# Optimization experiments

Hardware: AMD Instinct MI355X
Metric: run time of the kernel (lower is better)

Reference implementation:

```python
import math
import jax, jax.numpy as jnp
import numpy as np

DIM = 2048
N_HEADS = 16
HEAD_DIM = DIM // N_HEADS  # 128
BSZ = 2
SEQLEN = 2048
ROPE_THETA = 500000.0


def _make_freqs(seqlen, head_dim, theta):
    inv = 1.0 / (theta ** (np.arange(0, head_dim, 2, dtype=np.float32) / head_dim))
    t = np.arange(seqlen, dtype=np.float32)
    f = np.outer(t, inv)  # [S, hd//2]
    return jnp.asarray(np.cos(f)), jnp.asarray(np.sin(f))


def setup_inputs() -> dict:
    key = jax.random.key(0)
    kx, kq, kk, kv, ko = jax.random.split(key, 5)
    scale = 0.02
    x = jax.random.normal(kx, (BSZ, SEQLEN, DIM), dtype=jnp.float32)
    wq = jax.random.normal(kq, (DIM, DIM), dtype=jnp.float32) * scale
    wk = jax.random.normal(kk, (DIM, DIM), dtype=jnp.float32) * scale
    wv = jax.random.normal(kv, (DIM, DIM), dtype=jnp.float32) * scale
    wo = jax.random.normal(ko, (DIM, DIM), dtype=jnp.float32) * scale
    freqs_cos, freqs_sin = _make_freqs(SEQLEN, HEAD_DIM, ROPE_THETA)
    # causal additive mask: 0 on/below diag, -inf above
    mask = jnp.triu(jnp.full((SEQLEN, SEQLEN), float('-inf'), dtype=jnp.float32), k=1)
    return {"x": x, "start_pos": 0, "freqs_cos": freqs_cos, "freqs_sin": freqs_sin,
            "mask": mask, "wq": wq, "wk": wk, "wv": wv, "wo": wo}


def _apply_rope(t, cos, sin):
    # t: [B, S, H, hd]; cos/sin: [S, hd//2]
    b, s, h, hd = t.shape
    tr = t.reshape(b, s, h, hd // 2, 2)
    a, bb = tr[..., 0], tr[..., 1]
    c = cos[None, :, None, :]
    sn = sin[None, :, None, :]
    out_r = a * c - bb * sn
    out_i = a * sn + bb * c
    return jnp.stack([out_r, out_i], axis=-1).reshape(b, s, h, hd)


def reference(x, start_pos, freqs_cos, freqs_sin, mask, wq, wk, wv, wo):
    b, s, _ = x.shape
    xq = (x @ wq.T).reshape(b, s, N_HEADS, HEAD_DIM)
    xk = (x @ wk.T).reshape(b, s, N_HEADS, HEAD_DIM)
    xv = (x @ wv.T).reshape(b, s, N_HEADS, HEAD_DIM)
    xq = _apply_rope(xq, freqs_cos, freqs_sin)
    xk = _apply_rope(xk, freqs_cos, freqs_sin)
    # [B, H, S, hd]
    xq = xq.transpose(0, 2, 1, 3)
    xk = xk.transpose(0, 2, 1, 3)
    xv = xv.transpose(0, 2, 1, 3)
    scores = jnp.einsum('bhqd,bhkd->bhqk', xq, xk) / math.sqrt(HEAD_DIM)
    scores = scores + mask[None, None, :, :]
    probs = jax.nn.softmax(scores.astype(jnp.float32), axis=-1).astype(xq.dtype)
    out = jnp.einsum('bhqk,bhkd->bhqd', probs, xv)
    out = out.transpose(0, 2, 1, 3).reshape(b, s, -1)
    return out @ wo.T
```

## Files before the change

kernel.cpp:

```cpp
#include <hip/hip_runtime.h>
#include <stdint.h>

#define DIM 2048
#define SEQ 2048
#define NHEADS 16
#define HDIM 128
#define BSZ 2
#define ROWS (BSZ*SEQ)

typedef uint16_t u16;
typedef __attribute__((ext_vector_type(8))) short bf16x8;
typedef __attribute__((ext_vector_type(4))) float fx4;
typedef __attribute__((ext_vector_type(4))) uint16_t u16x4;

typedef const __attribute__((address_space(1))) uint32_t* gp_t;
typedef __attribute__((address_space(3))) uint32_t* lp_t;
#define GLL16(g, l) __builtin_amdgcn_global_load_lds((gp_t)(g), (lp_t)(l), 16, 0, 0)

__device__ inline u16 f2bf(float f) {
  union { float f; uint32_t u; } v; v.f = f;
  uint32_t u = v.u;
  u += 0x7FFFu + ((u >> 16) & 1u);
  return (u16)(u >> 16);
}
__device__ inline float bf2f(u16 h) {
  union { uint32_t u; float f; } v; v.u = ((uint32_t)h) << 16;
  return v.f;
}

__global__ __launch_bounds__(256) void cvt_kernel(const float* __restrict__ src,
                                                  u16* __restrict__ dst, int n4) {
  int i = blockIdx.x * 256 + threadIdx.x;
  if (i >= n4) return;
  fx4 f = *(const fx4*)(src + (size_t)i * 4);
  u16x4 o;
  o[0] = f2bf(f[0]); o[1] = f2bf(f[1]); o[2] = f2bf(f[2]); o[3] = f2bf(f[3]);
  *(u16x4*)(dst + (size_t)i * 4) = o;
}

__device__ inline void gemm128_core(const u16* __restrict__ A, const u16* __restrict__ B,
                                    u16 (&As)[128][32], u16 (&Bs)[128][32],
                                    fx4 (&acc)[4][4], int M0, int N0) {
  const int tid  = threadIdx.x;
  const int lane = tid & 63;
  const int wave = tid >> 6;
  const int wm = (wave >> 1) * 64;
  const int wn = (wave & 1) * 64;
  const int l16 = lane & 15;
  const int q8  = (lane >> 4) * 8;
#pragma unroll
  for (int tm = 0; tm < 4; ++tm)
#pragma unroll
    for (int tn = 0; tn < 4; ++tn) acc[tm][tn] = fx4{0.f, 0.f, 0.f, 0.f};

  const int wrow = wave * 32;
  const size_t laneA = (size_t)(M0 + wrow + (lane >> 2)) * DIM + (lane & 3) * 8;
  const size_t laneB = (size_t)(N0 + wrow + (lane >> 2)) * DIM + (lane & 3) * 8;

  for (int k0 = 0; k0 < DIM; k0 += 32) {
    __syncthreads();
    GLL16(A + laneA + k0,            &As[wrow][0]);
    GLL16(A + laneA + 16 * DIM + k0, &As[wrow + 16][0]);
    GLL16(B + laneB + k0,            &Bs[wrow][0]);
    GLL16(B + laneB + 16 * DIM + k0, &Bs[wrow + 16][0]);
    __syncthreads();
    bf16x8 af[4], bfr[4];
#pragma unroll
    for (int t = 0; t < 4; ++t) {
      af[t]  = *(const bf16x8*)&As[wm + t * 16 + l16][q8];
      bfr[t] = *(const bf16x8*)&Bs[wn + t * 16 + l16][q8];
    }
#pragma unroll
    for (int tm = 0; tm < 4; ++tm)
#pragma unroll
      for (int tn = 0; tn < 4; ++tn)
        acc[tm][tn] = __builtin_amdgcn_mfma_f32_16x16x32_bf16(af[tm], bfr[tn], acc[tm][tn], 0, 0, 0);
  }
}

__global__ __launch_bounds__(256) void gemm_qkv(const u16* __restrict__ A,
    const u16* __restrict__ B0, const u16* __restrict__ B1, const u16* __restrict__ B2,
    u16* __restrict__ C0, u16* __restrict__ C1, u16* __restrict__ C2) {
  __shared__ __align__(16) u16 As[128][32];
  __shared__ __align__(16) u16 Bs[128][32];
  const u16* B = (blockIdx.z == 0) ? B0 : (blockIdx.z == 1) ? B1 : B2;
  u16* C       = (blockIdx.z == 0) ? C0 : (blockIdx.z == 1) ? C1 : C2;
  const int M0 = blockIdx.y * 128, N0 = blockIdx.x * 128;
  fx4 acc[4][4];
  gemm128_core(A, B, As, Bs, acc, M0, N0);
  const int lane = threadIdx.x & 63, wave = threadIdx.x >> 6;
  const int wm = (wave >> 1) * 64, wn = (wave & 1) * 64;
  const int l16 = lane & 15, quad = lane >> 4;
#pragma unroll
  for (int tm = 0; tm < 4; ++tm)
#pragma unroll
    for (int tn = 0; tn < 4; ++tn)
#pragma unroll
      for (int r = 0; r < 4; ++r) {
        size_t row = (size_t)(M0 + wm + tm * 16 + quad * 4 + r);
        size_t col = (size_t)(N0 + wn + tn * 16 + l16);
        C[row * DIM + col] = f2bf(acc[tm][tn][r]);
      }
}

__global__ __launch_bounds__(256) void gemm_out(const u16* __restrict__ A,
                                                const u16* __restrict__ B,
                                                float* __restrict__ C) {
  __shared__ __align__(16) u16 As[128][32];
  __shared__ __align__(16) u16 Bs[128][32];
  const int M0 = blockIdx.y * 128, N0 = blockIdx.x * 128;
  fx4 acc[4][4];
  gemm128_core(A, B, As, Bs, acc, M0, N0);
  const int lane = threadIdx.x & 63, wave = threadIdx.x >> 6;
  const int wm = (wave >> 1) * 64, wn = (wave & 1) * 64;
  const int l16 = lane & 15, quad = lane >> 4;
#pragma unroll
  for (int tm = 0; tm < 4; ++tm)
#pragma unroll
    for (int tn = 0; tn < 4; ++tn)
#pragma unroll
      for (int r = 0; r < 4; ++r) {
        size_t row = (size_t)(M0 + wm + tm * 16 + quad * 4 + r);
        size_t col = (size_t)(N0 + wn + tn * 16 + l16);
        C[row * DIM + col] = acc[tm][tn][r];
      }
}

__global__ __launch_bounds__(256) void rope_kernel(u16* __restrict__ q, u16* __restrict__ k,
                                                   const float* __restrict__ fcos,
                                                   const float* __restrict__ fsin) {
  int idx = blockIdx.x * 256 + threadIdx.x;
  int t = idx >> 22;
  int p_all = idx & ((1 << 22) - 1);
  u16* ptr = t ? k : q;
  int row = p_all >> 10;
  int r   = p_all & 1023;
  int h   = r >> 6;
  int p   = r & 63;
  int s   = row & (SEQ - 1);
  size_t base = (size_t)row * DIM + h * HDIM + 2 * p;
  float a = bf2f(ptr[base]), b = bf2f(ptr[base + 1]);
  float c = fcos[s * 64 + p], sn = fsin[s * 64 + p];
  ptr[base]     = f2bf(a * c - b * sn);
  ptr[base + 1] = f2bf(a * sn + b * c);
}

__global__ __launch_bounds__(256) void vtrans_kernel(const u16* __restrict__ v,
                                                     u16* __restrict__ vtg) {
  __shared__ __align__(16) u16 T[128][72];
  const int tid = threadIdx.x;
  const int s0 = blockIdx.x * 64;
  const int bh = blockIdx.y;
  const int b = bh >> 4, h = bh & 15;
  const size_t vb = ((size_t)b * SEQ + s0) * DIM + h * HDIM;
#pragma unroll
  for (int i = 0; i < 4; ++i) {
    int c = i * 256 + tid;
    int s = c >> 4;
    int d0 = (c & 15) * 8;
    bf16x8 x = *(const bf16x8*)(v + vb + (size_t)s * DIM + d0);
#pragma unroll
    for (int j = 0; j < 8; ++j) T[d0 + j][s] = (u16)x[j];
  }
  __syncthreads();
  const size_t ob = ((size_t)bh * HDIM) * SEQ + s0;
#pragma unroll
  for (int i = 0; i < 4; ++i) {
    int c = i * 256 + tid;
    int d = c >> 3;
    int s8 = (c & 7) * 8;
    *(bf16x8*)(vtg + ob + (size_t)d * SEQ + s8) = *(const bf16x8*)&T[d][s8];
  }
}

__global__ __launch_bounds__(256) void attn_kernel(const u16* __restrict__ qm,
                                                   const u16* __restrict__ km,
                                                   const u16* __restrict__ vtg,
                                                   u16* __restrict__ ao) {
  __shared__ __align__(16) u16 Ks[64][136];
  __shared__ __align__(16) u16 Vt[128][72];
  __shared__ __align__(16) u16 Ps[4][16][72];
  const int tid = threadIdx.x;
  const int lane = tid & 63, wave = tid >> 6;
  const int l16 = lane & 15, quad = lane >> 4;
  const int bh = blockIdx.x;
  const int qt = (SEQ / 64 - 1) - blockIdx.y;
  const int b = bh >> 4, h = bh & 15;
  const int q0 = qt * 64;
  const size_t brow = (size_t)b * SEQ;
  const int hc = h * HDIM;
  const size_t vbase = (size_t)bh * HDIM * SEQ;

  bf16x8 aq[4];
  {
    size_t qbase = (brow + q0 + wave * 16 + l16) * DIM + hc;
#pragma unroll
    for (int dc = 0; dc < 4; ++dc)
      aq[dc] = *(const bf16x8*)(qm + qbase + dc * 32 + quad * 8);
  }
  fx4 o[8];
#pragma unroll
  for (int i = 0; i < 8; ++i) o[i] = fx4{0.f, 0.f, 0.f, 0.f};
  float mr[4], lr[4];
#pragma unroll
  for (int r = 0; r < 4; ++r) { mr[r] = -3e38f; lr[r] = 0.f; }

  bf16x8 kreg[4], vreg[4];
#pragma unroll
  for (int i = 0; i < 4; ++i) {
    int c = i * 256 + tid;
    kreg[i] = *(const bf16x8*)(km + (brow + (c >> 4)) * DIM + hc + (c & 15) * 8);
    vreg[i] = *(const bf16x8*)(vtg + vbase + (size_t)(c >> 3) * SEQ + (c & 7) * 8);
  }

  for (int kt = 0; kt <= qt; ++kt) {
    __syncthreads();
#pragma unroll
    for (int i = 0; i < 4; ++i) {
      int c = i * 256 + tid;
      *(bf16x8*)&Ks[c >> 4][(c & 15) * 8] = kreg[i];
      *(bf16x8*)&Vt[c >> 3][(c & 7) * 8] = vreg[i];
    }
    __syncthreads();
    if (kt < qt) {
      const int kv1 = (kt + 1) * 64;
#pragma unroll
      for (int i = 0; i < 4; ++i) {
        int c = i * 256 + tid;
        kreg[i] = *(const bf16x8*)(km + (brow + kv1 + (c >> 4)) * DIM + hc + (c & 15) * 8);
        vreg[i] = *(const bf16x8*)(vtg + vbase + (size_t)(c >> 3) * SEQ + kv1 + (c & 7) * 8);
      }
    }
    fx4 s[4];
#pragma unroll
    for (int tn = 0; tn < 4; ++tn) {
      fx4 acc = fx4{0.f, 0.f, 0.f, 0.f};
#pragma unroll
      for (int dc = 0; dc < 4; ++dc) {
        bf16x8 bk = *(const bf16x8*)&Ks[tn * 16 + l16][dc * 32 + quad * 8];
        acc = __builtin_amdgcn_mfma_f32_16x16x32_bf16(aq[dc], bk, acc, 0, 0, 0);
      }
      s[tn] = acc * 0.08838834764831845f;
    }
    if (kt == qt) {
      const int kv0 = kt * 64;
#pragma unroll
      for (int tn = 0; tn < 4; ++tn) {
        int kvpos = kv0 + tn * 16 + l16;
#pragma unroll
        for (int r = 0; r < 4; ++r) {
          int qpos = q0 + wave * 16 + quad * 4 + r;
          if (kvpos > qpos) s[tn][r] = -1e30f;
        }
      }
    }
    float alpha[4];
#pragma unroll
    for (int r = 0; r < 4; ++r) {
      float t = fmaxf(fmaxf(s[0][r], s[1][r]), fmaxf(s[2][r], s[3][r]));
      t = fmaxf(t, __shfl_xor(t, 1));
      t = fmaxf(t, __shfl_xor(t, 2));
      t = fmaxf(t, __shfl_xor(t, 4));
      t = fmaxf(t, __shfl_xor(t, 8));
      float mnew = fmaxf(mr[r], t);
      alpha[r] = __expf(mr[r] - mnew);
      float sm = 0.f;
#pragma unroll
      for (int tn = 0; tn < 4; ++tn) {
        float p = __expf(s[tn][r] - mnew);
        s[tn][r] = p;
        sm += p;
      }
      sm += __shfl_xor(sm, 1);
      sm += __shfl_xor(sm, 2);
      sm += __shfl_xor(sm, 4);
      sm += __shfl_xor(sm, 8);
      lr[r] = lr[r] * alpha[r] + sm;
      mr[r] = mnew;
    }
#pragma unroll
    for (int tn = 0; tn < 4; ++tn)
#pragma unroll
      for (int r = 0; r < 4; ++r)
        Ps[wave][quad * 4 + r][tn * 16 + l16] = f2bf(s[tn][r]);
#pragma unroll
    for (int nt = 0; nt < 8; ++nt) {
      fx4 t = o[nt];
      t[0] *= alpha[0]; t[1] *= alpha[1]; t[2] *= alpha[2]; t[3] *= alpha[3];
      o[nt] = t;
    }
#pragma unroll
    for (int t2 = 0; t2 < 2; ++t2) {
      bf16x8 ap = *(const bf16x8*)&Ps[wave][l16][t2 * 32 + quad * 8];
#pragma unroll
      for (int nt = 0; nt < 8; ++nt) {
        bf16x8 bv = *(const bf16x8*)&Vt[nt * 16 + l16][t2 * 32 + quad * 8];
        o[nt] = __builtin_amdgcn_mfma_f32_16x16x32_bf16(ap, bv, o[nt], 0, 0, 0);
      }
    }
  }
#pragma unroll
  for (int nt = 0; nt < 8; ++nt)
#pragma unroll
    for (int r = 0; r < 4; ++r) {
      float val = o[nt][r] / lr[r];
      size_t row = brow + q0 + wave * 16 + quad * 4 + r;
      ao[row * DIM + hc + nt * 16 + l16] = f2bf(val);
    }
}

extern "C" void kernel_launch(void* const* d_in, const int* in_sizes, int n_in,
                              void* d_out, int out_size, void* d_ws, size_t ws_size,
                              hipStream_t stream) {
  const float* x    = (const float*)d_in[0];
  const float* fcos = (const float*)d_in[2];
  const float* fsin = (const float*)d_in[3];
  const float* wq   = (const float*)d_in[5];
  const float* wk   = (const float*)d_in[6];
  const float* wv   = (const float*)d_in[7];
  const float* wo   = (const float*)d_in[8];
  float* out = (float*)d_out;

  const size_t XN = (size_t)ROWS * DIM;
  const size_t WN = (size_t)DIM * DIM;
  u16* ws  = (u16*)d_ws;
  u16* xb  = ws;
  u16* wqb = xb + XN;
  u16* wkb = wqb + WN;
  u16* wvb = wkb + WN;
  u16* wob = wvb + WN;
  u16* q   = wob + WN;
  u16* k   = q + XN;
  u16* v   = k + XN;
  u16* ao  = v + XN;
  u16* vtg = xb;

  cvt_kernel<<<(int)(XN / 4 / 256), 256, 0, stream>>>(x, xb, (int)(XN / 4));
  cvt_kernel<<<(int)(WN / 4 / 256), 256, 0, stream>>>(wq, wqb, (int)(WN / 4));
  cvt_kernel<<<(int)(WN / 4 / 256), 256, 0, stream>>>(wk, wkb, (int)(WN / 4));
  cvt_kernel<<<(int)(WN / 4 / 256), 256, 0, stream>>>(wv, wvb, (int)(WN / 4));
  cvt_kernel<<<(int)(WN / 4 / 256), 256, 0, stream>>>(wo, wob, (int)(WN / 4));

  gemm_qkv<<<dim3(DIM / 128, ROWS / 128, 3), 256, 0, stream>>>(xb, wqb, wkb, wvb, q, k, v);

  rope_kernel<<<2 * ROWS * 1024 / 256, 256, 0, stream>>>(q, k, fcos, fsin);
  vtrans_kernel<<<dim3(SEQ / 64, BSZ * NHEADS), 256, 0, stream>>>(v, vtg);

  attn_kernel<<<dim3(BSZ * NHEADS, SEQ / 64), 256, 0, stream>>>(q, k, vtg, ao);

  gemm_out<<<dim3(DIM / 128, ROWS / 128), 256, 0, stream>>>(ao, wob, out);
}
```

Baseline: 461.8 us.

## Enlarge attention Q tile to 128 rows with transposed MFMA and register P

The attention kernel now gives each block 128 query rows (32 per wave) instead of 64, with work interleaved so heavy and light causal tiles pair up. The QK product is computed transposed so P stays in registers and feeds a 16x16x16 MFMA directly, removing the P round-trip through shared memory. Output is staged through shared memory for coalesced stores. The five fp32-to-bf16 conversion launches are merged into one. The cost is more registers per thread and a new launch-bounds occupancy hint.

```diff
diff --git a/kernel.cpp b/kernel.cpp
--- a/kernel.cpp
+++ b/kernel.cpp
@@ -10,6 +10,7 @@
 
 typedef uint16_t u16;
 typedef __attribute__((ext_vector_type(8))) short bf16x8;
+typedef __attribute__((ext_vector_type(4))) short bf16x4;
 typedef __attribute__((ext_vector_type(4))) float fx4;
 typedef __attribute__((ext_vector_type(4))) uint16_t u16x4;
 
@@ -28,11 +29,23 @@
   return v.f;
 }
 
-__global__ __launch_bounds__(256) void cvt_kernel(const float* __restrict__ src,
-                                                  u16* __restrict__ dst, int n4) {
+__global__ __launch_bounds__(256) void cvt5_kernel(const float* __restrict__ sx,
+    const float* __restrict__ s1, const float* __restrict__ s2,
+    const float* __restrict__ s3, const float* __restrict__ s4,
+    u16* __restrict__ dst) {
+  const int XC = (ROWS * DIM) / 4;
+  const int WC = (DIM * DIM) / 4;
   int i = blockIdx.x * 256 + threadIdx.x;
-  if (i >= n4) return;
-  fx4 f = *(const fx4*)(src + (size_t)i * 4);
+  const float* src;
+  int off;
+  if (i < XC) { src = sx; off = i; }
+  else {
+    int t = i - XC;
+    int w = t >> 20;
+    off = t & (WC - 1);
+    src = (w == 0) ? s1 : (w == 1) ? s2 : (w == 2) ? s3 : s4;
+  }
+  fx4 f = *(const fx4*)(src + (size_t)off * 4);
   u16x4 o;
   o[0] = f2bf(f[0]); o[1] = f2bf(f[1]); o[2] = f2bf(f[2]); o[3] = f2bf(f[3]);
   *(u16x4*)(dst + (size_t)i * 4) = o;
@@ -173,37 +186,42 @@
   }
 }
 
-__global__ __launch_bounds__(256) void attn_kernel(const u16* __restrict__ qm,
-                                                   const u16* __restrict__ km,
-                                                   const u16* __restrict__ vtg,
-                                                   u16* __restrict__ ao) {
-  __shared__ __align__(16) u16 Ks[64][136];
-  __shared__ __align__(16) u16 Vt[128][72];
-  __shared__ __align__(16) u16 Ps[4][16][72];
+struct SMemS { u16 Ks[64][136]; u16 Vt[128][72]; };
+union SMemU { SMemS s; u16 Ot[4][32][136]; };
+
+__global__ __launch_bounds__(256, 2) void attn_kernel(const u16* __restrict__ qm,
+                                                      const u16* __restrict__ km,
+                                                      const u16* __restrict__ vtg,
+                                                      u16* __restrict__ ao) {
+  __shared__ __align__(16) SMemU sm;
   const int tid = threadIdx.x;
   const int lane = tid & 63, wave = tid >> 6;
   const int l16 = lane & 15, quad = lane >> 4;
-  const int bh = blockIdx.x;
-  const int qt = (SEQ / 64 - 1) - blockIdx.y;
+  const int idx = blockIdx.x;
+  const int bh = idx & 31;
+  const int j = idx >> 5;
+  const int qt = (j < 8) ? (15 - j) : (j - 8);
   const int b = bh >> 4, h = bh & 15;
-  const int q0 = qt * 64;
+  const int q0 = qt * 128;
   const size_t brow = (size_t)b * SEQ;
   const int hc = h * HDIM;
   const size_t vbase = (size_t)bh * HDIM * SEQ;
-
-  bf16x8 aq[4];
-  {
-    size_t qbase = (brow + q0 + wave * 16 + l16) * DIM + hc;
+  const int nkt = 2 * qt + 2;
+
+  bf16x8 aq[2][4];
+#pragma unroll
+  for (int nt = 0; nt < 2; ++nt) {
+    size_t qbase = (brow + q0 + wave * 32 + nt * 16 + l16) * DIM + hc;
 #pragma unroll
     for (int dc = 0; dc < 4; ++dc)
-      aq[dc] = *(const bf16x8*)(qm + qbase + dc * 32 + quad * 8);
-  }
-  fx4 o[8];
-#pragma unroll
-  for (int i = 0; i < 8; ++i) o[i] = fx4{0.f, 0.f, 0.f, 0.f};
-  float mr[4], lr[4];
-#pragma unroll
-  for (int r = 0; r < 4; ++r) { mr[r] = -3e38f; lr[r] = 0.f; }
+      aq[nt][dc] = *(const bf16x8*)(qm + qbase + dc * 32 + quad * 8);
+  }
+  fx4 o[2][8];
+#pragma unroll
+  for (int nt = 0; nt < 2; ++nt)
+#pragma unroll
+    for (int dt = 0; dt < 8; ++dt) o[nt][dt] = fx4{0.f, 0.f, 0.f, 0.f};
+  float mr[2] = {-3e38f, -3e38f}, lr[2] = {0.f, 0.f};
 
   bf16x8 kreg[4], vreg[4];
 #pragma unroll
@@ -213,16 +231,16 @@
     vreg[i] = *(const bf16x8*)(vtg + vbase + (size_t)(c >> 3) * SEQ + (c & 7) * 8);
   }
 
-  for (int kt = 0; kt <= qt; ++kt) {
+  for (int kt = 0; kt < nkt; ++kt) {
     __syncthreads();
 #pragma unroll
     for (int i = 0; i < 4; ++i) {
       int c = i * 256 + tid;
-      *(bf16x8*)&Ks[c >> 4][(c & 15) * 8] = kreg[i];
-      *(bf16x8*)&Vt[c >> 3][(c & 7) * 8] = vreg[i];
+      *(bf16x8*)&sm.s.Ks[c >> 4][(c & 15) * 8] = kreg[i];
+      *(bf16x8*)&sm.s.Vt[c >> 3][(c & 7) * 8] = vreg[i];
     }
     __syncthreads();
-    if (kt < qt) {
+    if (kt + 1 < nkt) {
       const int kv1 = (kt + 1) * 64;
 #pragma unroll
       for (int i = 0; i < 4; ++i) {
@@ -231,82 +249,96 @@
         vreg[i] = *(const bf16x8*)(vtg + vbase + (size_t)(c >> 3) * SEQ + kv1 + (c & 7) * 8);
       }
     }
-    fx4 s[4];
-#pragma unroll
-    for (int tn = 0; tn < 4; ++tn) {
-      fx4 acc = fx4{0.f, 0.f, 0.f, 0.f};
+    fx4 s[2][4];
+#pragma unroll
+    for (int tm = 0; tm < 4; ++tm) {
+      fx4 a0 = fx4{0.f, 0.f, 0.f, 0.f}, a1 = fx4{0.f, 0.f, 0.f, 0.f};
 #pragma unroll
       for (int dc = 0; dc < 4; ++dc) {
-        bf16x8 bk = *(const bf16x8*)&Ks[tn * 16 + l16][dc * 32 + quad * 8];
-        acc = __builtin_amdgcn_mfma_f32_16x16x32_bf16(aq[dc], bk, acc, 0, 0, 0);
-      }
-      s[tn] = acc * 0.08838834764831845f;
-    }
-    if (kt == qt) {
+        bf16x8 kf = *(const bf16x8*)&sm.s.Ks[tm * 16 + l16][dc * 32 + quad * 8];
+        a0 = __builtin_amdgcn_mfma_f32_16x16x32_bf16(kf, aq[0][dc], a0, 0, 0, 0);
+        a1 = __builtin_amdgcn_mfma_f32_16x16x32_bf16(kf, aq[1][dc], a1, 0, 0, 0);
+      }
+      s[0][tm] = a0 * 0.08838834764831845f;
+      s[1][tm] = a1 * 0.08838834764831845f;
+    }
+    if (kt >= nkt - 2) {
       const int kv0 = kt * 64;
 #pragma unroll
-      for (int tn = 0; tn < 4; ++tn) {
-        int kvpos = kv0 + tn * 16 + l16;
+      for (int nt = 0; nt < 2; ++nt) {
+        int qpos = q0 + wave * 32 + nt * 16 + l16;
+#pragma unroll
+        for (int tm = 0; tm < 4; ++tm)
+#pragma unroll
+          for (int r = 0; r < 4; ++r)
+            if (kv0 + tm * 16 + quad * 4 + r > qpos) s[nt][tm][r] = -1e30f;
+      }
+    }
+    float alpha[2];
+    bf16x4 pf[2][4];
+#pragma unroll
+    for (int nt = 0; nt < 2; ++nt) {
+      float t = -3e38f;
+#pragma unroll
+      for (int tm = 0; tm < 4; ++tm)
+        t = fmaxf(t, fmaxf(fmaxf(s[nt][tm][0], s[nt][tm][1]),
+                           fmaxf(s[nt][tm][2], s[nt][tm][3])));
+      t = fmaxf(t, __shfl_xor(t, 16));
+      t = fmaxf(t, __shfl_xor(t, 32));
+      float mnew = fmaxf(mr[nt], t);
+      alpha[nt] = __expf(mr[nt] - mnew);
+      float sum = 0.f;
+#pragma unroll
+      for (int tm = 0; tm < 4; ++tm) {
+        fx4 p;
 #pragma unroll
         for (int r = 0; r < 4; ++r) {
-          int qpos = q0 + wave * 16 + quad * 4 + r;
-          if (kvpos > qpos) s[tn][r] = -1e30f;
+          p[r] = __expf(s[nt][tm][r] - mnew);
+          sum += p[r];
         }
-      }
-    }
-    float alpha[4];
-#pragma unroll
-    for (int r = 0; r < 4; ++r) {
-      float t = fmaxf(fmaxf(s[0][r], s[1][r]), fmaxf(s[2][r], s[3][r]));
-      t = fmaxf(t, __shfl_xor(t, 1));
-      t = fmaxf(t, __shfl_xor(t, 2));
-      t = fmaxf(t, __shfl_xor(t, 4));
-      t = fmaxf(t, __shfl_xor(t, 8));
-      float mnew = fmaxf(mr[r], t);
-      alpha[r] = __expf(mr[r] - mnew);
-      float sm = 0.f;
-#pragma unroll
-      for (int tn = 0; tn < 4; ++tn) {
-        float p = __expf(s[tn][r] - mnew);
-        s[tn][r] = p;
-        sm += p;
-      }
-      sm += __shfl_xor(sm, 1);
-      sm += __shfl_xor(sm, 2);
-      sm += __shfl_xor(sm, 4);
-      sm += __shfl_xor(sm, 8);
-      lr[r] = lr[r] * alpha[r] + sm;
-      mr[r] = mnew;
-    }
-#pragma unroll
-    for (int tn = 0; tn < 4; ++tn)
-#pragma unroll
-      for (int r = 0; r < 4; ++r)
-        Ps[wave][quad * 4 + r][tn * 16 + l16] = f2bf(s[tn][r]);
-#pragma unroll
-    for (int nt = 0; nt < 8; ++nt) {
-      fx4 t = o[nt];
-      t[0] *= alpha[0]; t[1] *= alpha[1]; t[2] *= alpha[2]; t[3] *= alpha[3];
-      o[nt] = t;
-    }
-#pragma unroll
-    for (int t2 = 0; t2 < 2; ++t2) {
-      bf16x8 ap = *(const bf16x8*)&Ps[wave][l16][t2 * 32 + quad * 8];
-#pragma unroll
-      for (int nt = 0; nt < 8; ++nt) {
-        bf16x8 bv = *(const bf16x8*)&Vt[nt * 16 + l16][t2 * 32 + quad * 8];
-        o[nt] = __builtin_amdgcn_mfma_f32_16x16x32_bf16(ap, bv, o[nt], 0, 0, 0);
-      }
-    }
-  }
-#pragma unroll
-  for (int nt = 0; nt < 8; ++nt)
-#pragma unroll
-    for (int r = 0; r < 4; ++r) {
-      float val = o[nt][r] / lr[r];
-      size_t row = brow + q0 + wave * 16 + quad * 4 + r;
-      ao[row * DIM + hc + nt * 16 + l16] = f2bf(val);
-    }
+        bf16x4 pb;
+        pb[0] = (short)f2bf(p[0]); pb[1] = (short)f2bf(p[1]);
+        pb[2] = (short)f2bf(p[2]); pb[3] = (short)f2bf(p[3]);
+        pf[nt][tm] = pb;
+      }
+      sum += __shfl_xor(sum, 16);
+      sum += __shfl_xor(sum, 32);
+      lr[nt] = lr[nt] * alpha[nt] + sum;
+      mr[nt] = mnew;
+#pragma unroll
+      for (int dt = 0; dt < 8; ++dt) o[nt][dt] *= alpha[nt];
+    }
+#pragma unroll
+    for (int tm = 0; tm < 4; ++tm) {
+#pragma unroll
+      for (int dt = 0; dt < 8; ++dt) {
+        bf16x4 vf = *(const bf16x4*)&sm.s.Vt[dt * 16 + l16][tm * 16 + quad * 4];
+        o[0][dt] = __builtin_amdgcn_mfma_f32_16x16x16bf16_1k(vf, pf[0][tm], o[0][dt], 0, 0, 0);
+        o[1][dt] = __builtin_amdgcn_mfma_f32_16x16x16bf16_1k(vf, pf[1][tm], o[1][dt], 0, 0, 0);
+      }
+    }
+  }
+  __syncthreads();
+#pragma unroll
+  for (int nt = 0; nt < 2; ++nt) {
+    float inv = 1.f / lr[nt];
+#pragma unroll
+    for (int dt = 0; dt < 8; ++dt) {
+      fx4 v = o[nt][dt];
+      u16x4 p;
+      p[0] = f2bf(v[0] * inv); p[1] = f2bf(v[1] * inv);
+      p[2] = f2bf(v[2] * inv); p[3] = f2bf(v[3] * inv);
+      *(u16x4*)&sm.Ot[wave][nt * 16 + l16][dt * 16 + quad * 4] = p;
+    }
+  }
+#pragma unroll
+  for (int i = 0; i < 8; ++i) {
+    int c = i * 64 + lane;
+    int row = c >> 4;
+    int ch = c & 15;
+    bf16x8 t = *(const bf16x8*)&sm.Ot[wave][row][ch * 8];
+    *(bf16x8*)(ao + (brow + q0 + wave * 32 + row) * DIM + hc + ch * 8) = t;
+  }
 }
 
 extern "C" void kernel_launch(void* const* d_in, const int* in_sizes, int n_in,
@@ -335,18 +367,15 @@
   u16* ao  = v + XN;
   u16* vtg = xb;
 
-  cvt_kernel<<<(int)(XN / 4 / 256), 256, 0, stream>>>(x, xb, (int)(XN / 4));
-  cvt_kernel<<<(int)(WN / 4 / 256), 256, 0, stream>>>(wq, wqb, (int)(WN / 4));
-  cvt_kernel<<<(int)(WN / 4 / 256), 256, 0, stream>>>(wk, wkb, (int)(WN / 4));
-  cvt_kernel<<<(int)(WN / 4 / 256), 256, 0, stream>>>(wv, wvb, (int)(WN / 4));
-  cvt_kernel<<<(int)(WN / 4 / 256), 256, 0, stream>>>(wo, wob, (int)(WN / 4));
+  const int total_chunks = (int)((XN + 4 * WN) / 4);
+  cvt5_kernel<<<total_chunks / 256, 256, 0, stream>>>(x, wq, wk, wv, wo, ws);
 
   gemm_qkv<<<dim3(DIM / 128, ROWS / 128, 3), 256, 0, stream>>>(xb, wqb, wkb, wvb, q, k, v);
 
   rope_kernel<<<2 * ROWS * 1024 / 256, 256, 0, stream>>>(q, k, fcos, fsin);
   vtrans_kernel<<<dim3(SEQ / 64, BSZ * NHEADS), 256, 0, stream>>>(v, vtg);
 
-  attn_kernel<<<dim3(BSZ * NHEADS, SEQ / 64), 256, 0, stream>>>(q, k, vtg, ao);
+  attn_kernel<<<dim3(512), 256, 0, stream>>>(q, k, vtg, ao);
 
   gemm_out<<<dim3(DIM / 128, ROWS / 128), 256, 0, stream>>>(ao, wob, out);
 }
```

New measurement: 414.1 us. -10.3%, faster.
